# Optimization experiments

Measured on AMD Instinct MI355X. Metric: run time of the kernel, lower is better.

The kernel has to match this reference:

```python
import jax, jax.numpy as jnp
import numpy as np

EPS_NORM = 1e-12  # F.normalize eps
BN_EPS = 1e-5     # BatchNorm2d eps
N_NODES = 18
T_STEPS = 1280
FC_IN = 1469952


def _temporal_conv(x, wa, ba, wb, bb, wc, bc):
    """Gated temporal conv (GLU) from STConv's TemporalConv.
    x: (B, T, N, C) -> (B, T-k+1, N, Cout)."""
    xp = jnp.transpose(x, (0, 3, 2, 1))  # (B, C, N, T)

    def conv(w, b):
        y = jax.lax.conv_general_dilated(
            xp, w, window_strides=(1, 1), padding='VALID',
            dimension_numbers=('NCHW', 'OIHW', 'NCHW'))
        return y + b[None, :, None, None]

    P = conv(wa, ba)
    Q = jax.nn.sigmoid(conv(wb, bb))
    H = jax.nn.relu(P * Q + conv(wc, bc))
    return jnp.transpose(H, (0, 3, 2, 1))  # (B, T', N, Cout)


def setup_inputs() -> dict:
    key = jax.random.key(0)
    ks = jax.random.split(key, 16)
    s = 0.05
    inp = {
        'x': jax.random.normal(ks[0], (N_NODES, 1, T_STEPS), dtype=jnp.float32),
        'edge_index': jax.random.randint(ks[1], (2, 306), 0, N_NODES, dtype=jnp.int64),
        'edge_weight': jax.random.uniform(ks[2], (306,), dtype=jnp.float32),
        'w1a': jax.random.normal(ks[3], (64, 1, 1, 3), dtype=jnp.float32) * s,
        'b1a': jnp.zeros((64,), jnp.float32),
        'w1b': jax.random.normal(ks[4], (64, 1, 1, 3), dtype=jnp.float32) * s,
        'b1b': jnp.zeros((64,), jnp.float32),
        'w1c': jax.random.normal(ks[5], (64, 1, 1, 3), dtype=jnp.float32) * s,
        'b1c': jnp.zeros((64,), jnp.float32),
        'cheb_w': jax.random.normal(ks[6], (64, 64), dtype=jnp.float32) * s,
        'cheb_b': jnp.zeros((64,), jnp.float32),
        'w2a': jax.random.normal(ks[7], (64, 64, 1, 3), dtype=jnp.float32) * s,
        'b2a': jnp.zeros((64,), jnp.float32),
        'w2b': jax.random.normal(ks[8], (64, 64, 1, 3), dtype=jnp.float32) * s,
        'b2b': jnp.zeros((64,), jnp.float32),
        'w2c': jax.random.normal(ks[9], (64, 64, 1, 3), dtype=jnp.float32) * s,
        'b2c': jnp.zeros((64,), jnp.float32),
        'bn_gamma': jnp.ones((N_NODES,), jnp.float32),
        'bn_beta': jnp.zeros((N_NODES,), jnp.float32),
        'fc_w': jax.random.normal(ks[10], (1, FC_IN), dtype=jnp.float32) * 0.001,
        'fc_b': jnp.zeros((1,), jnp.float32),
    }
    return inp


def reference(x, edge_index, edge_weight,
              w1a, b1a, w1b, b1b, w1c, b1c,
              cheb_w, cheb_b,
              w2a, b2a, w2b, b2b, w2c, b2c,
              bn_gamma, bn_beta, fc_w, fc_b):
    # F.normalize(x, dim=1): x shape (N, 1, T)
    norm = jnp.sqrt(jnp.sum(x * x, axis=1, keepdims=True))
    xn = x / jnp.maximum(norm, EPS_NORM)
    # x[None].reshape([1, shape[3], shape[1], shape[2]]): row-major reshape (faithful)
    X = jnp.reshape(xn[None], (1, xn.shape[2], xn.shape[0], xn.shape[1]))  # (1, T, N, 1)

    T0 = _temporal_conv(X, w1a, b1a, w1b, b1b, w1c, b1c)  # (1, T-2, N, 64)
    # ChebConv with K=1: only T_0 = I term -> per-node linear; edge_index/edge_weight unused
    T = jnp.einsum('btnc,cd->btnd', T0, cheb_w) + cheb_b
    T = jax.nn.relu(T)
    T = _temporal_conv(T, w2a, b2a, w2b, b2b, w2c, b2c)  # (1, T-4, N, 64)

    # BatchNorm2d(num_nodes) in training mode: normalize per-node over (B, T, C)
    Tp = jnp.transpose(T, (0, 2, 1, 3))  # (B, N, T, C)
    mean = jnp.mean(Tp, axis=(0, 2, 3), keepdims=True)
    var = jnp.mean((Tp - mean) ** 2, axis=(0, 2, 3), keepdims=True)  # biased var
    Tn = (Tp - mean) / jnp.sqrt(var + BN_EPS)
    Tn = Tn * bn_gamma[None, :, None, None] + bn_beta[None, :, None, None]
    h = jnp.transpose(Tn, (0, 2, 1, 3))  # (B, T-4, N, C)

    h = jax.nn.relu(h).reshape(-1)  # flatten(start_dim=0)
    return fc_w @ h + fc_b  # (1,)
```

## Files before the change

### kernel.cpp

```cpp
#include <hip/hip_runtime.h>
#include <math.h>

#define NN 18
#define T_STEPS 1280
#define T1LEN 1278
#define T2LEN 1276
#define PREPBLK 144
#define TC2 62
#define NCHUNK2 ((T2LEN + TC2 - 1) / TC2)
#define NBLK (NCHUNK2 * NN)
#define DOT_BLOCKS 512

typedef __attribute__((ext_vector_type(8))) short short8;
typedef __attribute__((ext_vector_type(4))) float f32x4;

__device__ __forceinline__ unsigned short f2bf(float v) {
    unsigned u = __builtin_bit_cast(unsigned, v);
    u = u + 0x7fff + ((u >> 16) & 1);
    return (unsigned short)(u >> 16);
}
__device__ __forceinline__ float bf2f(unsigned short h) {
    unsigned u = ((unsigned)h) << 16;
    return __builtin_bit_cast(float, u);
}
__device__ __forceinline__ int swz(int row, int c) {
    return row * 64 + (((c >> 3) ^ (row & 7)) << 3) + (c & 7);
}

__global__ void k_wprep(const float* __restrict__ wa, const float* __restrict__ wb,
                        const float* __restrict__ wc,
                        unsigned short* __restrict__ WBhi, unsigned short* __restrict__ WBlo) {
    int i = blockIdx.x * 256 + threadIdx.x;
    if (i >= 6 * 192 * 32) return;
    int klocal = i & 31;
    int col = (i >> 5) % 192;
    int kb = i / (192 * 32);
    int conv = col >> 6, co = col & 63;
    int k = kb >> 1, ci = (kb & 1) * 32 + klocal;
    const float* w = (conv == 0) ? wa : (conv == 1 ? wb : wc);
    float v = w[co * 192 + ci * 3 + k];
    unsigned short hi = f2bf(v);
    WBhi[i] = hi;
    WBlo[i] = f2bf(v - bf2f(hi));
}

__global__ __launch_bounds__(256) void k_fuseall(const float* __restrict__ x,
        const float* __restrict__ w1a, const float* __restrict__ b1a,
        const float* __restrict__ w1b, const float* __restrict__ b1b,
        const float* __restrict__ w1c, const float* __restrict__ b1c,
        const float* __restrict__ cw, const float* __restrict__ cb,
        const unsigned short* __restrict__ WBhi, const unsigned short* __restrict__ WBlo,
        const float* __restrict__ b2a, const float* __restrict__ b2b,
        const float* __restrict__ b2c,
        float* __restrict__ T2, float* __restrict__ parts) {
    __shared__ float xs[66];
    __shared__ uint4 t1H[512], t1L[512];
    __shared__ uint4 t2H[528], t2L[528];
    __shared__ float red1[256], red2[256];
    int b = blockIdx.x;
    int node = b / NCHUNK2, chunk = b % NCHUNK2;
    int t0 = chunk * TC2;
    int tid = threadIdx.x;
    int l = tid & 63, w = tid >> 6;

    if (tid < 66) {
        int xt = t0 + tid;
        float v = (xt < T_STEPS) ? x[xt * NN + node] : 0.f;
        xs[tid] = v / fmaxf(fabsf(v), 1e-12f);
    }
    __syncthreads();

    {
        unsigned short* tH = (unsigned short*)t1H;
        unsigned short* tL = (unsigned short*)t1L;
        int c = l;
        float wa0 = w1a[c*3], wa1 = w1a[c*3+1], wa2 = w1a[c*3+2];
        float wb0 = w1b[c*3], wb1 = w1b[c*3+1], wb2 = w1b[c*3+2];
        float wc0 = w1c[c*3], wc1 = w1c[c*3+1], wc2 = w1c[c*3+2];
        float ba = b1a[c], bb = b1b[c], bc = b1c[c];
        #pragma unroll
        for (int j = 0; j < 16; ++j) {
            int r = w * 16 + j;
            float x0 = xs[r], x1 = xs[r + 1], x2 = xs[r + 2];
            float pa = fmaf(wa2, x2, fmaf(wa1, x1, fmaf(wa0, x0, ba)));
            float pb = fmaf(wb2, x2, fmaf(wb1, x1, fmaf(wb0, x0, bb)));
            float pc_ = fmaf(wc2, x2, fmaf(wc1, x1, fmaf(wc0, x0, bc)));
            float q = 1.0f / (1.0f + expf(-pb));
            float v = fmaxf(pa * q + pc_, 0.f);
            if (t0 + r >= T1LEN) v = 0.f;
            unsigned short hi = f2bf(v);
            int sw = swz(r, c);
            tH[sw] = hi;
            tL[sw] = f2bf(v - bf2f(hi));
        }
    }
    int d = w * 16 + (l & 15);
    short8 cbh[2], cbl[2];
    #pragma unroll
    for (int kb = 0; kb < 2; ++kb) {
        #pragma unroll
        for (int j = 0; j < 8; ++j) {
            float v = cw[(kb * 32 + (l >> 4) * 8 + j) * 64 + d];
            unsigned short hi = f2bf(v);
            cbh[kb][j] = (short)hi;
            cbl[kb][j] = (short)f2bf(v - bf2f(hi));
        }
    }
    __syncthreads();
    {
        f32x4 acc[4];
        #pragma unroll
        for (int mt = 0; mt < 4; ++mt) acc[mt] = (f32x4){0.f,0.f,0.f,0.f};
        #pragma unroll
        for (int kb = 0; kb < 2; ++kb) {
            #pragma unroll
            for (int mt = 0; mt < 4; ++mt) {
                int row = mt * 16 + (l & 15);
                int cbi = kb * 4 + (l >> 4);
                int si = row * 8 + (cbi ^ (row & 7));
                short8 ah = __builtin_bit_cast(short8, t1H[si]);
                short8 al = __builtin_bit_cast(short8, t1L[si]);
                acc[mt] = __builtin_amdgcn_mfma_f32_16x16x32_bf16(ah, cbh[kb], acc[mt], 0, 0, 0);
                acc[mt] = __builtin_amdgcn_mfma_f32_16x16x32_bf16(al, cbh[kb], acc[mt], 0, 0, 0);
                acc[mt] = __builtin_amdgcn_mfma_f32_16x16x32_bf16(ah, cbl[kb], acc[mt], 0, 0, 0);
            }
        }
        float cbias = cb[d];
        unsigned short* tH = (unsigned short*)t2H;
        unsigned short* tL = (unsigned short*)t2L;
        #pragma unroll
        for (int mt = 0; mt < 4; ++mt) {
            #pragma unroll
            for (int r = 0; r < 4; ++r) {
                int row = mt * 16 + (l >> 4) * 4 + r;
                float v = fmaxf(acc[mt][r] + cbias, 0.f);
                if (t0 + row >= T1LEN) v = 0.f;
                unsigned short hi = f2bf(v);
                int sw = swz(row, d);
                tH[sw] = hi;
                tL[sw] = f2bf(v - bf2f(hi));
            }
        }
        if (tid < 128) {
            int row = 64 + (tid >> 6), c = tid & 63;
            int sw = swz(row, c);
            tH[sw] = 0; tL[sw] = 0;
        }
    }
    __syncthreads();
    float s_sum = 0.f, s_sq = 0.f;
    {
        const uint4* wbh = (const uint4*)WBhi;
        const uint4* wbl = (const uint4*)WBlo;
        int co = w * 16 + (l & 15);
        f32x4 acc[4][3];
        #pragma unroll
        for (int mt = 0; mt < 4; ++mt)
            #pragma unroll
            for (int ct = 0; ct < 3; ++ct)
                acc[mt][ct] = (f32x4){0.f, 0.f, 0.f, 0.f};
        for (int kb = 0; kb < 6; ++kb) {
            short8 bh[3], bl[3];
            #pragma unroll
            for (int ct = 0; ct < 3; ++ct) {
                int col = (w + 4 * ct) * 16 + (l & 15);
                int gi = (kb * 192 + col) * 4 + (l >> 4);
                bh[ct] = __builtin_bit_cast(short8, wbh[gi]);
                bl[ct] = __builtin_bit_cast(short8, wbl[gi]);
            }
            #pragma unroll
            for (int mt = 0; mt < 4; ++mt) {
                int row = mt * 16 + (l & 15) + (kb >> 1);
                int cb2 = (kb & 1) * 4 + (l >> 4);
                int si = row * 8 + (cb2 ^ (row & 7));
                short8 ah = __builtin_bit_cast(short8, t2H[si]);
                short8 al = __builtin_bit_cast(short8, t2L[si]);
                acc[mt][0] = __builtin_amdgcn_mfma_f32_16x16x32_bf16(ah, bh[0], acc[mt][0], 0, 0, 0);
                acc[mt][1] = __builtin_amdgcn_mfma_f32_16x16x32_bf16(ah, bh[1], acc[mt][1], 0, 0, 0);
                acc[mt][2] = __builtin_amdgcn_mfma_f32_16x16x32_bf16(ah, bh[2], acc[mt][2], 0, 0, 0);
                acc[mt][0] = __builtin_amdgcn_mfma_f32_16x16x32_bf16(al, bh[0], acc[mt][0], 0, 0, 0);
                acc[mt][1] = __builtin_amdgcn_mfma_f32_16x16x32_bf16(al, bh[1], acc[mt][1], 0, 0, 0);
                acc[mt][2] = __builtin_amdgcn_mfma_f32_16x16x32_bf16(al, bh[2], acc[mt][2], 0, 0, 0);
                acc[mt][0] = __builtin_amdgcn_mfma_f32_16x16x32_bf16(ah, bl[0], acc[mt][0], 0, 0, 0);
                acc[mt][1] = __builtin_amdgcn_mfma_f32_16x16x32_bf16(ah, bl[1], acc[mt][1], 0, 0, 0);
                acc[mt][2] = __builtin_amdgcn_mfma_f32_16x16x32_bf16(ah, bl[2], acc[mt][2], 0, 0, 0);
            }
        }
        float ba = b2a[co], bb = b2b[co], bc = b2c[co];
        #pragma unroll
        for (int mt = 0; mt < 4; ++mt) {
            #pragma unroll
            for (int r = 0; r < 4; ++r) {
                int tl2 = mt * 16 + (l >> 4) * 4 + r;
                int t = t0 + tl2;
                if (tl2 < TC2 && t < T2LEN) {
                    float P = acc[mt][0][r] + ba, Q = acc[mt][1][r] + bb, Cc = acc[mt][2][r] + bc;
                    float qs = 1.f / (1.f + expf(-Q));
                    float hv = fmaxf(fmaf(P, qs, Cc), 0.f);
                    T2[(t * NN + node) * 64 + co] = hv;
                    s_sum += hv;
                    s_sq = fmaf(hv, hv, s_sq);
                }
            }
        }
    }
    red1[tid] = s_sum; red2[tid] = s_sq;
    __syncthreads();
    for (int off = 128; off > 0; off >>= 1) {
        if (tid < off) { red1[tid] += red1[tid + off]; red2[tid] += red2[tid + off]; }
        __syncthreads();
    }
    if (tid == 0) {
        parts[b * 2]     = red1[0];
        parts[b * 2 + 1] = red2[0];
    }
}

__global__ __launch_bounds__(256) void k_dot2(const float* __restrict__ T2,
        const float* __restrict__ parts,
        const float* __restrict__ gamma, const float* __restrict__ beta,
        const float* __restrict__ fcw, float* __restrict__ dpart) {
    __shared__ float sm[NN * 4];
    if (threadIdx.x < NN) {
        int n = threadIdx.x;
        float s = 0.f, q = 0.f;
        for (int i = 0; i < NCHUNK2; ++i) {
            s += parts[(n * NCHUNK2 + i) * 2];
            q += parts[(n * NCHUNK2 + i) * 2 + 1];
        }
        float cnt = (float)(T2LEN * 64);
        float mean = s / cnt;
        float var = q / cnt - mean * mean;
        sm[n * 4]     = mean;
        sm[n * 4 + 1] = rsqrtf(var + 1e-5f);
        sm[n * 4 + 2] = gamma[n];
        sm[n * 4 + 3] = beta[n];
    }
    __syncthreads();
    float acc = 0.f;
    const int total4 = T2LEN * NN * 64 / 4;
    const float4* T24 = (const float4*)T2;
    const float4* fw4 = (const float4*)fcw;
    for (int i = blockIdx.x * 256 + threadIdx.x; i < total4; i += DOT_BLOCKS * 256) {
        float4 t = T24[i];
        float4 f = fw4[i];
        int n = (i >> 4) % NN;
        float mu = sm[n * 4], is = sm[n * 4 + 1], g = sm[n * 4 + 2], bt = sm[n * 4 + 3];
        float v0 = fmaxf((t.x - mu) * is * g + bt, 0.f);
        float v1 = fmaxf((t.y - mu) * is * g + bt, 0.f);
        float v2 = fmaxf((t.z - mu) * is * g + bt, 0.f);
        float v3 = fmaxf((t.w - mu) * is * g + bt, 0.f);
        acc = fmaf(v0, f.x, acc);
        acc = fmaf(v1, f.y, acc);
        acc = fmaf(v2, f.z, acc);
        acc = fmaf(v3, f.w, acc);
    }
    __shared__ float r[256];
    r[threadIdx.x] = acc;
    __syncthreads();
    for (int off = 128; off > 0; off >>= 1) {
        if (threadIdx.x < off) r[threadIdx.x] += r[threadIdx.x + off];
        __syncthreads();
    }
    if (threadIdx.x == 0) dpart[blockIdx.x] = r[0];
}

__global__ __launch_bounds__(512) void k_final(const float* __restrict__ dpart,
                                               const float* __restrict__ fcb,
                                               float* __restrict__ out) {
    __shared__ float r[512];
    r[threadIdx.x] = dpart[threadIdx.x];
    __syncthreads();
    for (int off = 256; off > 0; off >>= 1) {
        if (threadIdx.x < off) r[threadIdx.x] += r[threadIdx.x + off];
        __syncthreads();
    }
    if (threadIdx.x == 0) out[0] = r[0] + fcb[0];
}

extern "C" void kernel_launch(void* const* d_in, const int* in_sizes, int n_in,
                              void* d_out, int out_size, void* d_ws, size_t ws_size,
                              hipStream_t stream) {
    const float* x     = (const float*)d_in[0];
    const float* w1a   = (const float*)d_in[3];
    const float* b1a   = (const float*)d_in[4];
    const float* w1b   = (const float*)d_in[5];
    const float* b1b   = (const float*)d_in[6];
    const float* w1c   = (const float*)d_in[7];
    const float* b1c   = (const float*)d_in[8];
    const float* chw   = (const float*)d_in[9];
    const float* chb   = (const float*)d_in[10];
    const float* w2a   = (const float*)d_in[11];
    const float* b2a   = (const float*)d_in[12];
    const float* w2b   = (const float*)d_in[13];
    const float* b2b   = (const float*)d_in[14];
    const float* w2c   = (const float*)d_in[15];
    const float* b2c   = (const float*)d_in[16];
    const float* gamma = (const float*)d_in[17];
    const float* beta  = (const float*)d_in[18];
    const float* fcw   = (const float*)d_in[19];
    const float* fcb   = (const float*)d_in[20];
    float* out = (float*)d_out;

    char* base = (char*)d_ws;
    float*          T2v   = (float*)(base);
    unsigned short* WBhi  = (unsigned short*)(base + 5879808);
    unsigned short* WBlo  = (unsigned short*)(base + 5953536);
    float*          parts = (float*)(base + 6027264);
    float*          dpart = (float*)(base + 6030336);

    k_wprep<<<PREPBLK, 256, 0, stream>>>(w2a, w2b, w2c, WBhi, WBlo);
    k_fuseall<<<NBLK, 256, 0, stream>>>(
        x, w1a, b1a, w1b, b1b, w1c, b1c, chw, chb,
        WBhi, WBlo, b2a, b2b, b2c, T2v, parts);
    k_dot2<<<DOT_BLOCKS, 256, 0, stream>>>(T2v, parts, gamma, beta, fcw, dpart);
    k_final<<<1, 512, 0, stream>>>(dpart, fcb, out);
}
```

Baseline: 30.87 us.

## Fold weight prep and final reduction into neighbouring kernels, enlarge time chunks

Removes the separate weight-prep kernel: each fused block now converts the second temporal-conv weights to hi/lo bf16 fragments held in registers. It also removes the final single-block reduction kernel, replacing it with a two-level last-block-done reduction using atomic counters inside the dot kernel. The time chunk per block grows from 62 to 92 rows, so there are fewer blocks and more MFMA work per block. The aim is to cut launch count and inter-kernel gaps. The cost is heavy register pressure from 36 short8 weight fragments plus 18 accumulators, redundant per-block weight conversion, and counter-reset ordering that relies on the previous kernel.

```diff
diff --git a/kernel.cpp b/kernel.cpp
--- a/kernel.cpp
+++ b/kernel.cpp
@@ -5,11 +5,11 @@
 #define T_STEPS 1280
 #define T1LEN 1278
 #define T2LEN 1276
-#define PREPBLK 144
-#define TC2 62
+#define TC2 92
 #define NCHUNK2 ((T2LEN + TC2 - 1) / TC2)
 #define NBLK (NCHUNK2 * NN)
 #define DOT_BLOCKS 512
+#define NGRP 32
 
 typedef __attribute__((ext_vector_type(8))) short short8;
 typedef __attribute__((ext_vector_type(4))) float f32x4;
@@ -27,43 +27,28 @@
     return row * 64 + (((c >> 3) ^ (row & 7)) << 3) + (c & 7);
 }
 
-__global__ void k_wprep(const float* __restrict__ wa, const float* __restrict__ wb,
-                        const float* __restrict__ wc,
-                        unsigned short* __restrict__ WBhi, unsigned short* __restrict__ WBlo) {
-    int i = blockIdx.x * 256 + threadIdx.x;
-    if (i >= 6 * 192 * 32) return;
-    int klocal = i & 31;
-    int col = (i >> 5) % 192;
-    int kb = i / (192 * 32);
-    int conv = col >> 6, co = col & 63;
-    int k = kb >> 1, ci = (kb & 1) * 32 + klocal;
-    const float* w = (conv == 0) ? wa : (conv == 1 ? wb : wc);
-    float v = w[co * 192 + ci * 3 + k];
-    unsigned short hi = f2bf(v);
-    WBhi[i] = hi;
-    WBlo[i] = f2bf(v - bf2f(hi));
-}
-
-__global__ __launch_bounds__(256) void k_fuseall(const float* __restrict__ x,
+__global__ __launch_bounds__(256) void k_fuse(const float* __restrict__ x,
         const float* __restrict__ w1a, const float* __restrict__ b1a,
         const float* __restrict__ w1b, const float* __restrict__ b1b,
         const float* __restrict__ w1c, const float* __restrict__ b1c,
         const float* __restrict__ cw, const float* __restrict__ cb,
-        const unsigned short* __restrict__ WBhi, const unsigned short* __restrict__ WBlo,
+        const float* __restrict__ w2a, const float* __restrict__ w2b,
+        const float* __restrict__ w2c,
         const float* __restrict__ b2a, const float* __restrict__ b2b,
         const float* __restrict__ b2c,
-        float* __restrict__ T2, float* __restrict__ parts) {
-    __shared__ float xs[66];
-    __shared__ uint4 t1H[512], t1L[512];
-    __shared__ uint4 t2H[528], t2L[528];
+        float* __restrict__ T2, float* __restrict__ parts, int* __restrict__ cnts) {
+    __shared__ float xs[104];
+    __shared__ uint4 t1H[768], t1L[768];
+    __shared__ uint4 t2H[784], t2L[784];
     __shared__ float red1[256], red2[256];
     int b = blockIdx.x;
     int node = b / NCHUNK2, chunk = b % NCHUNK2;
     int t0 = chunk * TC2;
     int tid = threadIdx.x;
     int l = tid & 63, w = tid >> 6;
-
-    if (tid < 66) {
+    if (b == 0 && tid < NGRP + 1) cnts[tid * 32] = 0;
+
+    if (tid < 98) {
         int xt = t0 + tid;
         float v = (xt < T_STEPS) ? x[xt * NN + node] : 0.f;
         xs[tid] = v / fmaxf(fabsf(v), 1e-12f);
@@ -79,8 +64,8 @@
         float wc0 = w1c[c*3], wc1 = w1c[c*3+1], wc2 = w1c[c*3+2];
         float ba = b1a[c], bb = b1b[c], bc = b1c[c];
         #pragma unroll
-        for (int j = 0; j < 16; ++j) {
-            int r = w * 16 + j;
+        for (int j = 0; j < 24; ++j) {
+            int r = w * 24 + j;
             float x0 = xs[r], x1 = xs[r + 1], x2 = xs[r + 2];
             float pa = fmaf(wa2, x2, fmaf(wa1, x1, fmaf(wa0, x0, ba)));
             float pb = fmaf(wb2, x2, fmaf(wb1, x1, fmaf(wb0, x0, bb)));
@@ -94,6 +79,27 @@
             tL[sw] = f2bf(v - bf2f(hi));
         }
     }
+
+    short8 bh[3][6], bl[3][6];
+    {
+        int co_b = w * 16 + (l & 15);
+        #pragma unroll
+        for (int ct = 0; ct < 3; ++ct) {
+            const float* wsrc = (ct == 0) ? w2a : (ct == 1 ? w2b : w2c);
+            #pragma unroll
+            for (int kb = 0; kb < 6; ++kb) {
+                int k = kb >> 1;
+                #pragma unroll
+                for (int j = 0; j < 8; ++j) {
+                    int ci = (kb & 1) * 32 + (l >> 4) * 8 + j;
+                    float v = wsrc[co_b * 192 + ci * 3 + k];
+                    unsigned short hi = f2bf(v);
+                    bh[ct][kb][j] = (short)hi;
+                    bl[ct][kb][j] = (short)f2bf(v - bf2f(hi));
+                }
+            }
+        }
+    }
     int d = w * 16 + (l & 15);
     short8 cbh[2], cbl[2];
     #pragma unroll
@@ -107,33 +113,34 @@
         }
     }
     __syncthreads();
+
     {
-        f32x4 acc[4];
-        #pragma unroll
-        for (int mt = 0; mt < 4; ++mt) acc[mt] = (f32x4){0.f,0.f,0.f,0.f};
+        f32x4 acc1[6];
+        #pragma unroll
+        for (int mt = 0; mt < 6; ++mt) acc1[mt] = (f32x4){0.f,0.f,0.f,0.f};
         #pragma unroll
         for (int kb = 0; kb < 2; ++kb) {
             #pragma unroll
-            for (int mt = 0; mt < 4; ++mt) {
+            for (int mt = 0; mt < 6; ++mt) {
                 int row = mt * 16 + (l & 15);
                 int cbi = kb * 4 + (l >> 4);
                 int si = row * 8 + (cbi ^ (row & 7));
                 short8 ah = __builtin_bit_cast(short8, t1H[si]);
                 short8 al = __builtin_bit_cast(short8, t1L[si]);
-                acc[mt] = __builtin_amdgcn_mfma_f32_16x16x32_bf16(ah, cbh[kb], acc[mt], 0, 0, 0);
-                acc[mt] = __builtin_amdgcn_mfma_f32_16x16x32_bf16(al, cbh[kb], acc[mt], 0, 0, 0);
-                acc[mt] = __builtin_amdgcn_mfma_f32_16x16x32_bf16(ah, cbl[kb], acc[mt], 0, 0, 0);
+                acc1[mt] = __builtin_amdgcn_mfma_f32_16x16x32_bf16(ah, cbh[kb], acc1[mt], 0, 0, 0);
+                acc1[mt] = __builtin_amdgcn_mfma_f32_16x16x32_bf16(al, cbh[kb], acc1[mt], 0, 0, 0);
+                acc1[mt] = __builtin_amdgcn_mfma_f32_16x16x32_bf16(ah, cbl[kb], acc1[mt], 0, 0, 0);
             }
         }
         float cbias = cb[d];
         unsigned short* tH = (unsigned short*)t2H;
         unsigned short* tL = (unsigned short*)t2L;
         #pragma unroll
-        for (int mt = 0; mt < 4; ++mt) {
+        for (int mt = 0; mt < 6; ++mt) {
             #pragma unroll
             for (int r = 0; r < 4; ++r) {
                 int row = mt * 16 + (l >> 4) * 4 + r;
-                float v = fmaxf(acc[mt][r] + cbias, 0.f);
+                float v = fmaxf(acc1[mt][r] + cbias, 0.f);
                 if (t0 + row >= T1LEN) v = 0.f;
                 unsigned short hi = f2bf(v);
                 int sw = swz(row, d);
@@ -142,53 +149,45 @@
             }
         }
         if (tid < 128) {
-            int row = 64 + (tid >> 6), c = tid & 63;
+            int row = 96 + (tid >> 6), c = tid & 63;
             int sw = swz(row, c);
             tH[sw] = 0; tL[sw] = 0;
         }
     }
     __syncthreads();
+
     float s_sum = 0.f, s_sq = 0.f;
     {
-        const uint4* wbh = (const uint4*)WBhi;
-        const uint4* wbl = (const uint4*)WBlo;
         int co = w * 16 + (l & 15);
-        f32x4 acc[4][3];
-        #pragma unroll
-        for (int mt = 0; mt < 4; ++mt)
+        f32x4 acc[6][3];
+        #pragma unroll
+        for (int mt = 0; mt < 6; ++mt)
             #pragma unroll
             for (int ct = 0; ct < 3; ++ct)
                 acc[mt][ct] = (f32x4){0.f, 0.f, 0.f, 0.f};
+        #pragma unroll
         for (int kb = 0; kb < 6; ++kb) {
-            short8 bh[3], bl[3];
-            #pragma unroll
-            for (int ct = 0; ct < 3; ++ct) {
-                int col = (w + 4 * ct) * 16 + (l & 15);
-                int gi = (kb * 192 + col) * 4 + (l >> 4);
-                bh[ct] = __builtin_bit_cast(short8, wbh[gi]);
-                bl[ct] = __builtin_bit_cast(short8, wbl[gi]);
-            }
-            #pragma unroll
-            for (int mt = 0; mt < 4; ++mt) {
+            #pragma unroll
+            for (int mt = 0; mt < 6; ++mt) {
                 int row = mt * 16 + (l & 15) + (kb >> 1);
                 int cb2 = (kb & 1) * 4 + (l >> 4);
                 int si = row * 8 + (cb2 ^ (row & 7));
                 short8 ah = __builtin_bit_cast(short8, t2H[si]);
                 short8 al = __builtin_bit_cast(short8, t2L[si]);
-                acc[mt][0] = __builtin_amdgcn_mfma_f32_16x16x32_bf16(ah, bh[0], acc[mt][0], 0, 0, 0);
-                acc[mt][1] = __builtin_amdgcn_mfma_f32_16x16x32_bf16(ah, bh[1], acc[mt][1], 0, 0, 0);
-                acc[mt][2] = __builtin_amdgcn_mfma_f32_16x16x32_bf16(ah, bh[2], acc[mt][2], 0, 0, 0);
-                acc[mt][0] = __builtin_amdgcn_mfma_f32_16x16x32_bf16(al, bh[0], acc[mt][0], 0, 0, 0);
-                acc[mt][1] = __builtin_amdgcn_mfma_f32_16x16x32_bf16(al, bh[1], acc[mt][1], 0, 0, 0);
-                acc[mt][2] = __builtin_amdgcn_mfma_f32_16x16x32_bf16(al, bh[2], acc[mt][2], 0, 0, 0);
-                acc[mt][0] = __builtin_amdgcn_mfma_f32_16x16x32_bf16(ah, bl[0], acc[mt][0], 0, 0, 0);
-                acc[mt][1] = __builtin_amdgcn_mfma_f32_16x16x32_bf16(ah, bl[1], acc[mt][1], 0, 0, 0);
-                acc[mt][2] = __builtin_amdgcn_mfma_f32_16x16x32_bf16(ah, bl[2], acc[mt][2], 0, 0, 0);
+                acc[mt][0] = __builtin_amdgcn_mfma_f32_16x16x32_bf16(ah, bh[0][kb], acc[mt][0], 0, 0, 0);
+                acc[mt][1] = __builtin_amdgcn_mfma_f32_16x16x32_bf16(ah, bh[1][kb], acc[mt][1], 0, 0, 0);
+                acc[mt][2] = __builtin_amdgcn_mfma_f32_16x16x32_bf16(ah, bh[2][kb], acc[mt][2], 0, 0, 0);
+                acc[mt][0] = __builtin_amdgcn_mfma_f32_16x16x32_bf16(al, bh[0][kb], acc[mt][0], 0, 0, 0);
+                acc[mt][1] = __builtin_amdgcn_mfma_f32_16x16x32_bf16(al, bh[1][kb], acc[mt][1], 0, 0, 0);
+                acc[mt][2] = __builtin_amdgcn_mfma_f32_16x16x32_bf16(al, bh[2][kb], acc[mt][2], 0, 0, 0);
+                acc[mt][0] = __builtin_amdgcn_mfma_f32_16x16x32_bf16(ah, bl[0][kb], acc[mt][0], 0, 0, 0);
+                acc[mt][1] = __builtin_amdgcn_mfma_f32_16x16x32_bf16(ah, bl[1][kb], acc[mt][1], 0, 0, 0);
+                acc[mt][2] = __builtin_amdgcn_mfma_f32_16x16x32_bf16(ah, bl[2][kb], acc[mt][2], 0, 0, 0);
             }
         }
         float ba = b2a[co], bb = b2b[co], bc = b2c[co];
         #pragma unroll
-        for (int mt = 0; mt < 4; ++mt) {
+        for (int mt = 0; mt < 6; ++mt) {
             #pragma unroll
             for (int r = 0; r < 4; ++r) {
                 int tl2 = mt * 16 + (l >> 4) * 4 + r;
@@ -216,13 +215,17 @@
     }
 }
 
-__global__ __launch_bounds__(256) void k_dot2(const float* __restrict__ T2,
+__global__ __launch_bounds__(256) void k_dotfin(const float* __restrict__ T2,
         const float* __restrict__ parts,
         const float* __restrict__ gamma, const float* __restrict__ beta,
-        const float* __restrict__ fcw, float* __restrict__ dpart) {
+        const float* __restrict__ fcw, const float* __restrict__ fcb,
+        float* dpart, float* gdot, int* cnts, float* __restrict__ out) {
     __shared__ float sm[NN * 4];
-    if (threadIdx.x < NN) {
-        int n = threadIdx.x;
+    __shared__ float r[256];
+    __shared__ int lastGrp, lastAll;
+    int tid = threadIdx.x;
+    if (tid < NN) {
+        int n = tid;
         float s = 0.f, q = 0.f;
         for (int i = 0; i < NCHUNK2; ++i) {
             s += parts[(n * NCHUNK2 + i) * 2];
@@ -241,7 +244,7 @@
     const int total4 = T2LEN * NN * 64 / 4;
     const float4* T24 = (const float4*)T2;
     const float4* fw4 = (const float4*)fcw;
-    for (int i = blockIdx.x * 256 + threadIdx.x; i < total4; i += DOT_BLOCKS * 256) {
+    for (int i = blockIdx.x * 256 + tid; i < total4; i += DOT_BLOCKS * 256) {
         float4 t = T24[i];
         float4 f = fw4[i];
         int n = (i >> 4) % NN;
@@ -255,27 +258,39 @@
         acc = fmaf(v2, f.z, acc);
         acc = fmaf(v3, f.w, acc);
     }
-    __shared__ float r[256];
-    r[threadIdx.x] = acc;
+    r[tid] = acc;
     __syncthreads();
     for (int off = 128; off > 0; off >>= 1) {
-        if (threadIdx.x < off) r[threadIdx.x] += r[threadIdx.x + off];
+        if (tid < off) r[tid] += r[tid + off];
         __syncthreads();
     }
-    if (threadIdx.x == 0) dpart[blockIdx.x] = r[0];
-}
-
-__global__ __launch_bounds__(512) void k_final(const float* __restrict__ dpart,
-                                               const float* __restrict__ fcb,
-                                               float* __restrict__ out) {
-    __shared__ float r[512];
-    r[threadIdx.x] = dpart[threadIdx.x];
-    __syncthreads();
-    for (int off = 256; off > 0; off >>= 1) {
-        if (threadIdx.x < off) r[threadIdx.x] += r[threadIdx.x + off];
-        __syncthreads();
-    }
-    if (threadIdx.x == 0) out[0] = r[0] + fcb[0];
+    int b = blockIdx.x;
+    int grp = b >> 4;
+    if (tid == 0) {
+        __hip_atomic_store(&dpart[b], r[0], __ATOMIC_RELEASE, __HIP_MEMORY_SCOPE_AGENT);
+        int o = __hip_atomic_fetch_add(&cnts[grp * 32], 1, __ATOMIC_ACQ_REL, __HIP_MEMORY_SCOPE_AGENT);
+        lastGrp = (o == 15);
+    }
+    __syncthreads();
+    if (!lastGrp) return;
+    if (tid == 0) {
+        float s = 0.f;
+        #pragma unroll
+        for (int i = 0; i < 16; ++i)
+            s += __hip_atomic_load(&dpart[grp * 16 + i], __ATOMIC_ACQUIRE, __HIP_MEMORY_SCOPE_AGENT);
+        __hip_atomic_store(&gdot[grp], s, __ATOMIC_RELEASE, __HIP_MEMORY_SCOPE_AGENT);
+        int o2 = __hip_atomic_fetch_add(&cnts[NGRP * 32], 1, __ATOMIC_ACQ_REL, __HIP_MEMORY_SCOPE_AGENT);
+        lastAll = (o2 == NGRP - 1);
+    }
+    __syncthreads();
+    if (!lastAll) return;
+    if (tid == 0) {
+        float s = 0.f;
+        #pragma unroll
+        for (int g = 0; g < NGRP; ++g)
+            s += __hip_atomic_load(&gdot[g], __ATOMIC_ACQUIRE, __HIP_MEMORY_SCOPE_AGENT);
+        out[0] = s + fcb[0];
+    }
 }
 
 extern "C" void kernel_launch(void* const* d_in, const int* in_sizes, int n_in,
@@ -303,16 +318,15 @@
     float* out = (float*)d_out;
 
     char* base = (char*)d_ws;
-    float*          T2v   = (float*)(base);
-    unsigned short* WBhi  = (unsigned short*)(base + 5879808);
-    unsigned short* WBlo  = (unsigned short*)(base + 5953536);
-    float*          parts = (float*)(base + 6027264);
-    float*          dpart = (float*)(base + 6030336);
-
-    k_wprep<<<PREPBLK, 256, 0, stream>>>(w2a, w2b, w2c, WBhi, WBlo);
-    k_fuseall<<<NBLK, 256, 0, stream>>>(
+    float* T2v   = (float*)(base);
+    float* parts = (float*)(base + 5879808);
+    float* dpart = (float*)(base + 5881856);
+    float* gdot  = (float*)(base + 5883904);
+    int*   cnts  = (int*)(base + 5884032);
+
+    k_fuse<<<NBLK, 256, 0, stream>>>(
         x, w1a, b1a, w1b, b1b, w1c, b1c, chw, chb,
-        WBhi, WBlo, b2a, b2b, b2c, T2v, parts);
-    k_dot2<<<DOT_BLOCKS, 256, 0, stream>>>(T2v, parts, gamma, beta, fcw, dpart);
-    k_final<<<1, 512, 0, stream>>>(dpart, fcb, out);
-}
+        w2a, w2b, w2c, b2a, b2b, b2c, T2v, parts, cnts);
+    k_dotfin<<<DOT_BLOCKS, 256, 0, stream>>>(
+        T2v, parts, gamma, beta, fcw, fcb, dpart, gdot, cnts, out);
+}
```

Result: slower. 54.96 us (+78.0%).
